# Kernel optimization log

Hardware: AMD Instinct MI355X
Metric: run time of the kernel (lower is better)

Reference implementation:

```python
import jax, jax.numpy as jnp
import numpy as np

B, S, D, T = 64, 1024, 768, 10
IS = int(S * 0.3)   # 307, token-mix inner dim
ID = int(D * 0.3)   # 230, channel-mix inner dim
EPS = 1e-5


def _cond_ln(x, embed, tid):
    # LayerNorm over last dim (no affine), then per-sample gamma/beta
    mu = jnp.mean(x, axis=-1, keepdims=True)
    var = jnp.mean(jnp.square(x - mu), axis=-1, keepdims=True)
    out = (x - mu) / jnp.sqrt(var + EPS)
    gb = embed[tid]                      # [B, 2D]
    gamma, beta = gb[:, :D], gb[:, D:]
    return gamma[:, None, :] * out + beta[:, None, :]


def setup_inputs() -> dict:
    key = jax.random.key(0)
    ks = jax.random.split(key, 8)
    x = jax.random.normal(ks[0], (B, S, D), dtype=jnp.float32)
    tasks_id = jax.random.randint(ks[1], (B,), 0, T)
    # conditional LN embeddings: gamma ~ N(1, 0.02), beta = 0
    cln1 = jnp.concatenate([1.0 + 0.02 * jax.random.normal(ks[2], (T, D)),
                            jnp.zeros((T, D))], axis=1).astype(jnp.float32)
    cln2 = jnp.concatenate([1.0 + 0.02 * jax.random.normal(ks[3], (T, D)),
                            jnp.zeros((T, D))], axis=1).astype(jnp.float32)
    # per-task weights stored [T, fout, fin] (kaiming-ish scale)
    w1_tok = jax.random.normal(ks[4], (T, IS, S), dtype=jnp.float32) * (2.0 / S) ** 0.5
    w2_tok = jax.random.normal(ks[5], (T, S, IS), dtype=jnp.float32) * (2.0 / IS) ** 0.5
    w1_ch = jax.random.normal(ks[6], (T, ID, D), dtype=jnp.float32) * (2.0 / D) ** 0.5
    w2_ch = jax.random.normal(ks[7], (T, D, ID), dtype=jnp.float32) * (2.0 / ID) ** 0.5
    return {"x": x, "tasks_id": tasks_id, "cln1": cln1, "cln2": cln2,
            "w1_tok": w1_tok, "w2_tok": w2_tok, "w1_ch": w1_ch, "w2_ch": w2_ch}


def reference(x, tasks_id, cln1, cln2, w1_tok, w2_tok, w1_ch, w2_ch):
    tid = tasks_id
    # --- token-mixing block (axis=1 ConditionalLinear) ---
    h = _cond_ln(x, cln1, tid)
    h = jnp.einsum('bnd,bcn->bcd', h, w1_tok[tid])   # [B, IS, D]
    h = jax.nn.gelu(h, approximate=False)
    h = jnp.einsum('bnd,bcn->bcd', h, w2_tok[tid])   # [B, S, D]
    x = x + h
    # --- channel-mixing block (axis=2 ConditionalLinear) ---
    h = _cond_ln(x, cln2, tid)
    h = jnp.einsum('bnd,bcd->bnc', h, w1_ch[tid])    # [B, S, ID]
    h = jax.nn.gelu(h, approximate=False)
    h = jnp.einsum('bnd,bcd->bnc', h, w2_ch[tid])    # [B, S, D]
    x = x + h
    return x
```

## Files before the change

kernel.cpp:

```cpp
#include <hip/hip_runtime.h>
#include <math.h>

typedef __bf16 bf16x8 __attribute__((ext_vector_type(8)));
typedef __bf16 bf16x4 __attribute__((ext_vector_type(4)));
typedef float  f32x4  __attribute__((ext_vector_type(4)));

constexpr int Bc = 64, Sc = 1024, Dc = 768;
constexpr int ISc = 307, IDc = 230;
constexpr int ISp = 384, IDp = 256;

static __device__ __forceinline__ float bf2f(unsigned short u) {
    return __builtin_bit_cast(float, (unsigned)u << 16);
}

static __device__ __forceinline__ void gload16(const void* g, void* l) {
    __builtin_amdgcn_global_load_lds(
        (const __attribute__((address_space(1))) void*)g,
        (__attribute__((address_space(3))) void*)l, 16, 0, 0);
}

constexpr int CH0 = 10 * ISp * (Sc  / 8);
constexpr int CH1 = 10 * Sc  * (ISp / 8);
constexpr int CH2 = 10 * IDp * (Dc  / 8);
constexpr int CH3 = 10 * Dc  * (IDp / 8);
constexpr int CB0 = CH0, CB1 = CB0 + CH1, CB2 = CB1 + CH2, CB3 = CB2 + CH3;

__device__ __forceinline__ void cvt_one(
    const float* __restrict__ in, __bf16* __restrict__ out,
    int inrows, int outrows, int incols, int outcols, int c)
{
    const int cpr  = outcols >> 3;
    const int perT = outrows * cpr;
    const int t    = c / perT;
    const int rem  = c - t * perT;
    const int r    = rem / cpr;
    const int cc   = (rem - r * cpr) * 8;
    bf16x8 o;
    if (r < inrows) {
        const float* src = in + ((long)t * inrows + r) * incols + cc;
        #pragma unroll
        for (int e = 0; e < 8; e++)
            o[e] = (cc + e < incols) ? (__bf16)src[e] : (__bf16)0.0f;
    } else {
        #pragma unroll
        for (int e = 0; e < 8; e++) o[e] = (__bf16)0.0f;
    }
    *reinterpret_cast<bf16x8*>(out + ((long)t * outrows + r) * outcols + cc) = o;
}

__global__ __launch_bounds__(256) void cvt_all(
    const float* __restrict__ w1t, const float* __restrict__ w2t,
    const float* __restrict__ w1c, const float* __restrict__ w2c,
    __bf16* __restrict__ o1t, __bf16* __restrict__ o2t,
    __bf16* __restrict__ o1c, __bf16* __restrict__ o2c)
{
    const int c = blockIdx.x * 256 + threadIdx.x;
    if (c < CB0)      cvt_one(w1t, o1t, ISc, ISp, Sc,  Sc,  c);
    else if (c < CB1) cvt_one(w2t, o2t, Sc,  Sc,  ISc, ISp, c - CB0);
    else if (c < CB2) cvt_one(w1c, o1c, IDc, IDp, Dc,  Dc,  c - CB1);
    else if (c < CB3) cvt_one(w2c, o2c, Dc,  Dc,  IDc, IDp, c - CB2);
}

__global__ __launch_bounds__(256) void ln1_t(
    const float* __restrict__ x, const int* __restrict__ tasks,
    const float* __restrict__ cln, __bf16* __restrict__ h1T)
{
    constexpr int RPB = 32, LDT = Dc + 8;
    __shared__ unsigned short T[RPB * LDT];
    const int b   = blockIdx.y;
    const int t   = tasks[b];
    const int s0  = blockIdx.x * RPB;
    const int tid = threadIdx.x;
    const int wv  = tid >> 6;
    const int l   = tid & 63;

    const float4* Ga = reinterpret_cast<const float4*>(cln + (long)t * 2 * Dc);
    const float4* Be = reinterpret_cast<const float4*>(cln + (long)t * 2 * Dc + Dc);
    const float4 g0 = Ga[l], g1 = Ga[l + 64], g2 = Ga[l + 128];
    const float4 b0 = Be[l], b1 = Be[l + 64], b2 = Be[l + 128];

    #pragma unroll
    for (int rr = 0; rr < 8; rr++) {
        const int r = wv * 8 + rr;
        const float4* xr = reinterpret_cast<const float4*>(x + ((long)b * Sc + s0 + r) * Dc);
        const float4 v0 = xr[l], v1 = xr[l + 64], v2 = xr[l + 128];
        float s = v0.x + v0.y + v0.z + v0.w + v1.x + v1.y + v1.z + v1.w
                + v2.x + v2.y + v2.z + v2.w;
        float q = v0.x*v0.x + v0.y*v0.y + v0.z*v0.z + v0.w*v0.w
                + v1.x*v1.x + v1.y*v1.y + v1.z*v1.z + v1.w*v1.w
                + v2.x*v2.x + v2.y*v2.y + v2.z*v2.z + v2.w*v2.w;
        #pragma unroll
        for (int o = 1; o < 64; o <<= 1) { s += __shfl_xor(s, o); q += __shfl_xor(q, o); }
        const float mu   = s * (1.0f / Dc);
        const float var  = fmaxf(q * (1.0f / Dc) - mu * mu, 0.0f);
        const float rstd = 1.0f / sqrtf(var + 1e-5f);
        unsigned short* tr = &T[r * LDT];
        bf16x4 o0, o1, o2;
        o0[0] = (__bf16)(g0.x * ((v0.x - mu) * rstd) + b0.x);
        o0[1] = (__bf16)(g0.y * ((v0.y - mu) * rstd) + b0.y);
        o0[2] = (__bf16)(g0.z * ((v0.z - mu) * rstd) + b0.z);
        o0[3] = (__bf16)(g0.w * ((v0.w - mu) * rstd) + b0.w);
        o1[0] = (__bf16)(g1.x * ((v1.x - mu) * rstd) + b1.x);
        o1[1] = (__bf16)(g1.y * ((v1.y - mu) * rstd) + b1.y);
        o1[2] = (__bf16)(g1.z * ((v1.z - mu) * rstd) + b1.z);
        o1[3] = (__bf16)(g1.w * ((v1.w - mu) * rstd) + b1.w);
        o2[0] = (__bf16)(g2.x * ((v2.x - mu) * rstd) + b2.x);
        o2[1] = (__bf16)(g2.y * ((v2.y - mu) * rstd) + b2.y);
        o2[2] = (__bf16)(g2.z * ((v2.z - mu) * rstd) + b2.z);
        o2[3] = (__bf16)(g2.w * ((v2.w - mu) * rstd) + b2.w);
        *reinterpret_cast<bf16x4*>(&tr[l * 4])        = o0;
        *reinterpret_cast<bf16x4*>(&tr[256 + l * 4])  = o1;
        *reinterpret_cast<bf16x4*>(&tr[512 + l * 4])  = o2;
    }
    __syncthreads();
    #pragma unroll
    for (int c = 0; c < 3; c++) {
        const int d = tid + c * 256;
        unsigned short tmp[32];
        #pragma unroll
        for (int e = 0; e < 32; e++) tmp[e] = T[e * LDT + d];
        __bf16* dst = h1T + ((long)b * Dc + d) * Sc + s0;
        #pragma unroll
        for (int u = 0; u < 4; u++)
            reinterpret_cast<uint4*>(dst)[u] = reinterpret_cast<const uint4*>(tmp)[u];
    }
}

__global__ __launch_bounds__(256) void cond_ln_b(
    const __bf16* __restrict__ x, const int* __restrict__ tasks,
    const float* __restrict__ cln, __bf16* __restrict__ out)
{
    const int row = blockIdx.x * 4 + (threadIdx.x >> 6);
    const int b   = row >> 10;
    const int t   = tasks[b];
    const int l   = threadIdx.x & 63;
    const ushort4* xr = reinterpret_cast<const ushort4*>(x + (long)row * Dc);
    const ushort4 u0 = xr[l], u1 = xr[l + 64], u2 = xr[l + 128];
    float v[12];
    v[0]=bf2f(u0.x); v[1]=bf2f(u0.y); v[2]=bf2f(u0.z); v[3]=bf2f(u0.w);
    v[4]=bf2f(u1.x); v[5]=bf2f(u1.y); v[6]=bf2f(u1.z); v[7]=bf2f(u1.w);
    v[8]=bf2f(u2.x); v[9]=bf2f(u2.y); v[10]=bf2f(u2.z); v[11]=bf2f(u2.w);
    float s = 0.f, q = 0.f;
    #pragma unroll
    for (int e = 0; e < 12; e++) { s += v[e]; q += v[e] * v[e]; }
    #pragma unroll
    for (int o = 1; o < 64; o <<= 1) { s += __shfl_xor(s, o); q += __shfl_xor(q, o); }
    const float mu   = s * (1.0f / Dc);
    const float var  = fmaxf(q * (1.0f / Dc) - mu * mu, 0.0f);
    const float rstd = 1.0f / sqrtf(var + 1e-5f);
    const float4* Ga = reinterpret_cast<const float4*>(cln + (long)t * 2 * Dc);
    const float4* Be = reinterpret_cast<const float4*>(cln + (long)t * 2 * Dc + Dc);
    ushort4* orow = reinterpret_cast<ushort4*>(out + (long)row * Dc);
    #pragma unroll
    for (int c = 0; c < 3; c++) {
        const float4 g = Ga[l + c * 64], be = Be[l + c * 64];
        bf16x4 o;
        o[0] = (__bf16)(g.x * ((v[c*4+0] - mu) * rstd) + be.x);
        o[1] = (__bf16)(g.y * ((v[c*4+1] - mu) * rstd) + be.y);
        o[2] = (__bf16)(g.z * ((v[c*4+2] - mu) * rstd) + be.z);
        o[3] = (__bf16)(g.w * ((v[c*4+3] - mu) * rstd) + be.w);
        orow[l + c * 64] = __builtin_bit_cast(ushort4, o);
    }
}

template<int DOGELU, int RESM, int OUTF32, int ATASK>
__global__ __launch_bounds__(256, 2) void gemm_tn(
    const __bf16* __restrict__ A, long sA, int lda,
    const __bf16* __restrict__ B, long sB, int ldb,
    const void* __restrict__ R, long sR,
    void* __restrict__ C, long sC, int ldc,
    const int* __restrict__ tasks, int M, int N, int K)
{
    constexpr int BM = 128, BN = 128, BK = 64;
    constexpr int BUFB = 32768;
    __shared__ uint4 lds4[2 * BUFB / 16];
    char* lbase = (char*)lds4;

    const int gx  = gridDim.x, gy = gridDim.y;
    const int tpb = gx * gy;
    const long lin = blockIdx.x + (long)gx * (blockIdx.y + (long)gy * blockIdx.z);
    const int  xcd  = (int)(lin & 7);
    const long idx  = lin >> 3;
    const int  lb   = (int)(idx / tpb);
    const int  tile = (int)(idx - (long)lb * tpb);
    const int  b    = xcd * 8 + lb;
    const int  m0   = (tile / gx) * BM;
    const int  n0   = (tile % gx) * BN;

    const int t = tasks[b];
    const __bf16* Ab = A + (ATASK ? (long)t : (long)b) * sA;
    const __bf16* Bb = B + (ATASK ? (long)b : (long)t) * sB;
    const int tid = threadIdx.x, lane = tid & 63, wid = tid >> 6;
    const int wm = (wid >> 1) * 64, wn = (wid & 1) * 64;
    const int l15 = lane & 15, l4 = lane >> 4;

    f32x4 acc[4][4];
    #pragma unroll
    for (int i = 0; i < 4; i++)
        #pragma unroll
        for (int j = 0; j < 4; j++)
            acc[i][j] = (f32x4){0.f, 0.f, 0.f, 0.f};

    auto STAGE = [&](int k0, int buf) {
        char* dst = lbase + buf * BUFB;
        #pragma unroll
        for (int rep = 0; rep < 4; rep++) {
            const int c = rep * 256 + tid;
            const int m = c >> 3, ch = c & 7;
            const int gk = k0 + ((ch ^ (m & 7)) << 3);
            gload16(Ab + (long)(m0 + m) * lda + gk, dst + c * 16);
        }
        #pragma unroll
        for (int rep = 0; rep < 4; rep++) {
            const int c = rep * 256 + tid;
            const int n = c >> 3, ch = c & 7;
            const int gk = k0 + ((ch ^ (n & 7)) << 3);
            gload16(Bb + (long)(n0 + n) * ldb + gk, dst + 16384 + c * 16);
        }
    };

    const int nt = K / BK;
    STAGE(0, 0);
    __syncthreads();
    int cur = 0;
    for (int tt = 0; tt < nt; tt++) {
        if (tt + 1 < nt) STAGE((tt + 1) * BK, cur ^ 1);
        const char* bb = lbase + cur * BUFB;
        #pragma unroll
        for (int h = 0; h < 2; h++) {
            bf16x8 af[4], bfr[4];
            #pragma unroll
            for (int i = 0; i < 4; i++) {
                const int row = wm + i * 16 + l15;
                af[i] = *reinterpret_cast<const bf16x8*>(
                    bb + row * 128 + (((h * 4 + l4) ^ (l15 & 7)) << 4));
            }
            #pragma unroll
            for (int j = 0; j < 4; j++) {
                const int row = wn + j * 16 + l15;
                bfr[j] = *reinterpret_cast<const bf16x8*>(
                    bb + 16384 + row * 128 + (((h * 4 + l4) ^ (l15 & 7)) << 4));
            }
            #pragma unroll
            for (int i = 0; i < 4; i++)
                #pragma unroll
                for (int j = 0; j < 4; j++)
                    acc[i][j] = __builtin_amdgcn_mfma_f32_16x16x32_bf16(af[i], bfr[j], acc[i][j], 0, 0, 0);
        }
        __syncthreads();
        cur ^= 1;
    }

    float*  Cf = (float*)C  + (long)b * sC;
    __bf16* Ch = (__bf16*)C + (long)b * sC;
    const float*  Rf = (RESM == 1) ? ((const float*)R  + (long)b * sR) : nullptr;
    const __bf16* Rh = (RESM == 2) ? ((const __bf16*)R + (long)b * sR) : nullptr;

    #pragma unroll
    for (int i = 0; i < 4; i++) {
        #pragma unroll
        for (int j = 0; j < 4; j++) {
            const int gn = n0 + wn + j * 16 + l15;
            #pragma unroll
            for (int r = 0; r < 4; r++) {
                const int gm = m0 + wm + i * 16 + l4 * 4 + r;
                float v = acc[i][j][r];
                if (DOGELU) v = 0.5f * v * (1.0f + erff(v * 0.70710678118654752f));
                if (RESM == 1) v += Rf[(long)gm * ldc + gn];
                if (RESM == 2) v += (float)Rh[(long)gm * ldc + gn];
                if (OUTF32) Cf[(long)gm * ldc + gn] = v;
                else        Ch[(long)gm * ldc + gn] = (__bf16)v;
            }
        }
    }
}

extern "C" void kernel_launch(void* const* d_in, const int* in_sizes, int n_in,
                              void* d_out, int out_size, void* d_ws, size_t ws_size,
                              hipStream_t stream) {
    const float* x      = (const float*)d_in[0];
    const int*   tasks  = (const int*)  d_in[1];
    const float* cln1   = (const float*)d_in[2];
    const float* cln2   = (const float*)d_in[3];
    const float* w1_tok = (const float*)d_in[4];
    const float* w2_tok = (const float*)d_in[5];
    const float* w1_ch  = (const float*)d_in[6];
    const float* w2_ch  = (const float*)d_in[7];
    float* out = (float*)d_out;

    char* ws = (char*)d_ws;
    const long oT1 = 0;
    const long oT2 = oT1 + (long)10 * ISp * Sc * 2;
    const long oC1 = oT2 + (long)10 * Sc * ISp * 2;
    const long oC2 = oC1 + (long)10 * IDp * Dc * 2;
    const long oA  = oC2 + (long)10 * Dc * IDp * 2;
    const long oG  = oA  + (long)Bc * Dc * Sc * 2;
    __bf16* wT1  = (__bf16*)(ws + oT1);
    __bf16* wT2  = (__bf16*)(ws + oT2);
    __bf16* wC1  = (__bf16*)(ws + oC1);
    __bf16* wC2  = (__bf16*)(ws + oC2);
    __bf16* h1T  = (__bf16*)(ws + oA);
    __bf16* x1   = (__bf16*)(ws + oA);
    __bf16* gbf  = (__bf16*)(ws + oG);
    __bf16* h2   = (__bf16*)d_out;

    const dim3 blk(256);
    auto cdiv = [](long a, long b) { return (int)((a + b - 1) / b); };

    cvt_all<<<cdiv(CB3, 256), blk, 0, stream>>>(
        w1_tok, w2_tok, w1_ch, w2_ch, wT1, wT2, wC1, wC2);

    ln1_t<<<dim3(Sc / 32, Bc), blk, 0, stream>>>(x, tasks, cln1, h1T);

    gemm_tn<1, 0, 0, 0><<<dim3(ISp / 128, Dc / 128, Bc), blk, 0, stream>>>(
        h1T, (long)Dc * Sc, Sc,
        wT1, (long)ISp * Sc, Sc,
        nullptr, 0,
        gbf, (long)Dc * ISp, ISp,
        tasks, Dc, ISp, Sc);

    gemm_tn<0, 1, 0, 1><<<dim3(Dc / 128, Sc / 128, Bc), blk, 0, stream>>>(
        wT2, (long)Sc * ISp, ISp,
        gbf, (long)Dc * ISp, ISp,
        x, (long)Sc * Dc,
        x1, (long)Sc * Dc, Dc,
        tasks, Sc, Dc, ISp);

    cond_ln_b<<<(Bc * Sc) / 4, blk, 0, stream>>>(x1, tasks, cln2, h2);

    gemm_tn<1, 0, 0, 0><<<dim3(IDp / 128, Sc / 128, Bc), blk, 0, stream>>>(
        h2, (long)Sc * Dc, Dc,
        wC1, (long)IDp * Dc, Dc,
        nullptr, 0,
        gbf, (long)Sc * IDp, IDp,
        tasks, Sc, IDp, Dc);

    gemm_tn<0, 2, 1, 0><<<dim3(Dc / 128, Sc / 128, Bc), blk, 0, stream>>>(
        gbf, (long)Sc * IDp, IDp,
        wC2, (long)Dc * IDp, IDp,
        x1, (long)Sc * Dc,
        out, (long)Sc * Dc, Dc,
        tasks, Sc, Dc, IDp);
}
```

Before: 461.3 us.

## Fuse channel-mix LayerNorm, both GEMMs, GELU and residual into one kernel

```diff
diff --git a/kernel.cpp b/kernel.cpp
--- a/kernel.cpp
+++ b/kernel.cpp
@@ -11,6 +11,9 @@
 
 static __device__ __forceinline__ float bf2f(unsigned short u) {
     return __builtin_bit_cast(float, (unsigned)u << 16);
+}
+static __device__ __forceinline__ float gelu_f(float v) {
+    return 0.5f * v * (1.0f + erff(v * 0.70710678118654752f));
 }
 
 static __device__ __forceinline__ void gload16(const void* g, void* l) {
@@ -126,43 +129,6 @@
     }
 }
 
-__global__ __launch_bounds__(256) void cond_ln_b(
-    const __bf16* __restrict__ x, const int* __restrict__ tasks,
-    const float* __restrict__ cln, __bf16* __restrict__ out)
-{
-    const int row = blockIdx.x * 4 + (threadIdx.x >> 6);
-    const int b   = row >> 10;
-    const int t   = tasks[b];
-    const int l   = threadIdx.x & 63;
-    const ushort4* xr = reinterpret_cast<const ushort4*>(x + (long)row * Dc);
-    const ushort4 u0 = xr[l], u1 = xr[l + 64], u2 = xr[l + 128];
-    float v[12];
-    v[0]=bf2f(u0.x); v[1]=bf2f(u0.y); v[2]=bf2f(u0.z); v[3]=bf2f(u0.w);
-    v[4]=bf2f(u1.x); v[5]=bf2f(u1.y); v[6]=bf2f(u1.z); v[7]=bf2f(u1.w);
-    v[8]=bf2f(u2.x); v[9]=bf2f(u2.y); v[10]=bf2f(u2.z); v[11]=bf2f(u2.w);
-    float s = 0.f, q = 0.f;
-    #pragma unroll
-    for (int e = 0; e < 12; e++) { s += v[e]; q += v[e] * v[e]; }
-    #pragma unroll
-    for (int o = 1; o < 64; o <<= 1) { s += __shfl_xor(s, o); q += __shfl_xor(q, o); }
-    const float mu   = s * (1.0f / Dc);
-    const float var  = fmaxf(q * (1.0f / Dc) - mu * mu, 0.0f);
-    const float rstd = 1.0f / sqrtf(var + 1e-5f);
-    const float4* Ga = reinterpret_cast<const float4*>(cln + (long)t * 2 * Dc);
-    const float4* Be = reinterpret_cast<const float4*>(cln + (long)t * 2 * Dc + Dc);
-    ushort4* orow = reinterpret_cast<ushort4*>(out + (long)row * Dc);
-    #pragma unroll
-    for (int c = 0; c < 3; c++) {
-        const float4 g = Ga[l + c * 64], be = Be[l + c * 64];
-        bf16x4 o;
-        o[0] = (__bf16)(g.x * ((v[c*4+0] - mu) * rstd) + be.x);
-        o[1] = (__bf16)(g.y * ((v[c*4+1] - mu) * rstd) + be.y);
-        o[2] = (__bf16)(g.z * ((v[c*4+2] - mu) * rstd) + be.z);
-        o[3] = (__bf16)(g.w * ((v[c*4+3] - mu) * rstd) + be.w);
-        orow[l + c * 64] = __builtin_bit_cast(ushort4, o);
-    }
-}
-
 template<int DOGELU, int RESM, int OUTF32, int ATASK>
 __global__ __launch_bounds__(256, 2) void gemm_tn(
     const __bf16* __restrict__ A, long sA, int lda,
@@ -233,13 +199,13 @@
             for (int i = 0; i < 4; i++) {
                 const int row = wm + i * 16 + l15;
                 af[i] = *reinterpret_cast<const bf16x8*>(
-                    bb + row * 128 + (((h * 4 + l4) ^ (l15 & 7)) << 4));
+                    bb + row * 128 + (((h * 4 + l4) ^ (row & 7)) << 4));
             }
             #pragma unroll
             for (int j = 0; j < 4; j++) {
                 const int row = wn + j * 16 + l15;
                 bfr[j] = *reinterpret_cast<const bf16x8*>(
-                    bb + 16384 + row * 128 + (((h * 4 + l4) ^ (l15 & 7)) << 4));
+                    bb + 16384 + row * 128 + (((h * 4 + l4) ^ (row & 7)) << 4));
             }
             #pragma unroll
             for (int i = 0; i < 4; i++)
@@ -265,11 +231,223 @@
             for (int r = 0; r < 4; r++) {
                 const int gm = m0 + wm + i * 16 + l4 * 4 + r;
                 float v = acc[i][j][r];
-                if (DOGELU) v = 0.5f * v * (1.0f + erff(v * 0.70710678118654752f));
+                if (DOGELU) v = gelu_f(v);
                 if (RESM == 1) v += Rf[(long)gm * ldc + gn];
                 if (RESM == 2) v += (float)Rh[(long)gm * ldc + gn];
                 if (OUTF32) Cf[(long)gm * ldc + gn] = v;
                 else        Ch[(long)gm * ldc + gn] = (__bf16)v;
+            }
+        }
+    }
+}
+
+__global__ __launch_bounds__(512, 1) void mlp_ch(
+    const __bf16* __restrict__ x1, const int* __restrict__ tasks,
+    const float* __restrict__ cln2,
+    const __bf16* __restrict__ wC1,
+    const __bf16* __restrict__ wC2,
+    float* __restrict__ out)
+{
+    __shared__ float2 st[128];
+    __shared__ unsigned short G[128 * 256];
+    __shared__ char sbuf[2][32768];
+
+    const int lin = blockIdx.x;
+    const int xcd = lin & 7;
+    const int idx = lin >> 3;
+    const int b   = xcd * 8 + (idx >> 3);
+    const int m0  = (idx & 7) * 128;
+    const int t   = tasks[b];
+
+    const int tid = threadIdx.x;
+    const int wid = tid >> 6, lane = tid & 63;
+    const int g   = wid >> 2, wid2 = wid & 3;
+    const int wm  = (wid2 >> 1) * 64, wn = (wid2 & 1) * 64;
+    const int l15 = lane & 15, l4 = lane >> 4;
+
+    const __bf16* xb = x1 + ((long)b * Sc + m0) * Dc;
+    const float*  cg = cln2 + (long)t * 2 * Dc;
+    const float*  cb = cg + Dc;
+
+    #pragma unroll 2
+    for (int rr = 0; rr < 16; rr++) {
+        const int m = wid * 16 + rr;
+        const ushort4* xr = reinterpret_cast<const ushort4*>(xb + (long)m * Dc);
+        const ushort4 u0 = xr[lane], u1 = xr[lane + 64], u2 = xr[lane + 128];
+        float s = 0.f, q = 0.f, v;
+        v = bf2f(u0.x); s += v; q += v*v;  v = bf2f(u0.y); s += v; q += v*v;
+        v = bf2f(u0.z); s += v; q += v*v;  v = bf2f(u0.w); s += v; q += v*v;
+        v = bf2f(u1.x); s += v; q += v*v;  v = bf2f(u1.y); s += v; q += v*v;
+        v = bf2f(u1.z); s += v; q += v*v;  v = bf2f(u1.w); s += v; q += v*v;
+        v = bf2f(u2.x); s += v; q += v*v;  v = bf2f(u2.y); s += v; q += v*v;
+        v = bf2f(u2.z); s += v; q += v*v;  v = bf2f(u2.w); s += v; q += v*v;
+        #pragma unroll
+        for (int o = 1; o < 64; o <<= 1) { s += __shfl_xor(s, o); q += __shfl_xor(q, o); }
+        if (lane == 0) {
+            const float mu  = s * (1.0f / Dc);
+            const float var = fmaxf(q * (1.0f / Dc) - mu * mu, 0.0f);
+            st[m] = make_float2(mu, 1.0f / sqrtf(var + 1e-5f));
+        }
+    }
+    __syncthreads();
+
+    const int am = tid >> 2, ach = tid & 3;
+    const float2 ams = st[am];
+    const __bf16* arow = xb + (long)am * Dc;
+
+    auto loadA = [&](int kt) -> bf16x8 {
+        return *reinterpret_cast<const bf16x8*>(arow + kt * 32 + ach * 8);
+    };
+    auto writeA = [&](bf16x8 a, int buf) {
+        const int gk = 0;  (void)gk;
+        *reinterpret_cast<bf16x8*>(sbuf[buf] + am * 64 + ((ach ^ (am & 3)) << 4)) = a;
+    };
+    auto stageB1 = [&](int kt, int buf) {
+        #pragma unroll
+        for (int rep = 0; rep < 2; rep++) {
+            const int c = rep * 512 + tid;
+            const int n = c >> 2, ch = c & 3;
+            const int gk = kt * 32 + ((ch ^ (n & 3)) << 3);
+            gload16(wC1 + ((long)t * IDp + n) * Dc + gk, sbuf[buf] + 8192 + c * 16);
+        }
+    };
+    auto xformA = [&](bf16x8 raw, int kt) -> bf16x8 {
+        const int gk = kt * 32 + ach * 8;
+        const float4 ga0 = reinterpret_cast<const float4*>(cg + gk)[0];
+        const float4 ga1 = reinterpret_cast<const float4*>(cg + gk)[1];
+        const float4 be0 = reinterpret_cast<const float4*>(cb + gk)[0];
+        const float4 be1 = reinterpret_cast<const float4*>(cb + gk)[1];
+        bf16x8 o;
+        o[0] = (__bf16)(ga0.x * ((float)raw[0] - ams.x) * ams.y + be0.x);
+        o[1] = (__bf16)(ga0.y * ((float)raw[1] - ams.x) * ams.y + be0.y);
+        o[2] = (__bf16)(ga0.z * ((float)raw[2] - ams.x) * ams.y + be0.z);
+        o[3] = (__bf16)(ga0.w * ((float)raw[3] - ams.x) * ams.y + be0.w);
+        o[4] = (__bf16)(ga1.x * ((float)raw[4] - ams.x) * ams.y + be1.x);
+        o[5] = (__bf16)(ga1.y * ((float)raw[5] - ams.x) * ams.y + be1.y);
+        o[6] = (__bf16)(ga1.z * ((float)raw[6] - ams.x) * ams.y + be1.z);
+        o[7] = (__bf16)(ga1.w * ((float)raw[7] - ams.x) * ams.y + be1.w);
+        return o;
+    };
+
+    f32x4 acc[4][4];
+    #pragma unroll
+    for (int i = 0; i < 4; i++)
+        #pragma unroll
+        for (int j = 0; j < 4; j++)
+            acc[i][j] = (f32x4){0.f, 0.f, 0.f, 0.f};
+
+    {
+        bf16x8 a0 = loadA(0);
+        stageB1(0, 0);
+        writeA(xformA(a0, 0), 0);
+        __syncthreads();
+        for (int kt = 0; kt < 24; kt++) {
+            const int buf = kt & 1;
+            bf16x8 anx;
+            if (kt < 23) { anx = loadA(kt + 1); stageB1(kt + 1, buf ^ 1); }
+            const char* Abase = sbuf[buf];
+            const char* Bbase = sbuf[buf] + 8192;
+            bf16x8 af[4], bfr[4];
+            #pragma unroll
+            for (int i = 0; i < 4; i++) {
+                const int row = wm + i * 16 + l15;
+                af[i] = *reinterpret_cast<const bf16x8*>(
+                    Abase + row * 64 + ((l4 ^ (row & 3)) << 4));
+            }
+            #pragma unroll
+            for (int j = 0; j < 4; j++) {
+                const int row = g * 128 + wn + j * 16 + l15;
+                bfr[j] = *reinterpret_cast<const bf16x8*>(
+                    Bbase + row * 64 + ((l4 ^ (row & 3)) << 4));
+            }
+            #pragma unroll
+            for (int i = 0; i < 4; i++)
+                #pragma unroll
+                for (int j = 0; j < 4; j++)
+                    acc[i][j] = __builtin_amdgcn_mfma_f32_16x16x32_bf16(af[i], bfr[j], acc[i][j], 0, 0, 0);
+            if (kt < 23) writeA(xformA(anx, kt + 1), buf ^ 1);
+            __syncthreads();
+        }
+    }
+
+    #pragma unroll
+    for (int i = 0; i < 4; i++) {
+        #pragma unroll
+        for (int j = 0; j < 4; j++) {
+            const int k = g * 128 + wn + j * 16 + l15;
+            #pragma unroll
+            for (int r = 0; r < 4; r++) {
+                const int m = wm + i * 16 + l4 * 4 + r;
+                const float v = gelu_f(acc[i][j][r]);
+                const int chunk = k >> 3;
+                const int phys  = chunk ^ (m & 7);
+                G[m * 256 + phys * 8 + (k & 7)] =
+                    __builtin_bit_cast(unsigned short, (__bf16)v);
+            }
+        }
+    }
+    __syncthreads();
+
+    const __bf16* w2b = wC2 + (long)t * Dc * IDp;
+    for (int nc = 0; nc < 3; nc++) {
+        auto stageB2 = [&](int kt, int buf) {
+            #pragma unroll
+            for (int rep = 0; rep < 4; rep++) {
+                const int c = rep * 512 + tid;
+                const int n = c >> 3, ch = c & 7;
+                const int gk = kt * 64 + ((ch ^ (n & 7)) << 3);
+                gload16(w2b + (long)(nc * 256 + n) * IDp + gk, sbuf[buf] + c * 16);
+            }
+        };
+        f32x4 a2[4][4];
+        #pragma unroll
+        for (int i = 0; i < 4; i++)
+            #pragma unroll
+            for (int j = 0; j < 4; j++)
+                a2[i][j] = (f32x4){0.f, 0.f, 0.f, 0.f};
+
+        stageB2(0, 0);
+        __syncthreads();
+        for (int kt = 0; kt < 4; kt++) {
+            const int buf = kt & 1;
+            if (kt < 3) stageB2(kt + 1, buf ^ 1);
+            #pragma unroll
+            for (int h = 0; h < 2; h++) {
+                bf16x8 af[4], bfr[4];
+                #pragma unroll
+                for (int i = 0; i < 4; i++) {
+                    const int row = wm + i * 16 + l15;
+                    const int chunk = kt * 8 + h * 4 + l4;
+                    const int phys  = chunk ^ (row & 7);
+                    af[i] = *reinterpret_cast<const bf16x8*>(
+                        (const char*)G + row * 512 + phys * 16);
+                }
+                #pragma unroll
+                for (int j = 0; j < 4; j++) {
+                    const int row = g * 128 + wn + j * 16 + l15;
+                    bfr[j] = *reinterpret_cast<const bf16x8*>(
+                        sbuf[buf] + row * 128 + (((h * 4 + l4) ^ (row & 7)) << 4));
+                }
+                #pragma unroll
+                for (int i = 0; i < 4; i++)
+                    #pragma unroll
+                    for (int j = 0; j < 4; j++)
+                        a2[i][j] = __builtin_amdgcn_mfma_f32_16x16x32_bf16(af[i], bfr[j], a2[i][j], 0, 0, 0);
+            }
+            __syncthreads();
+        }
+        float* ob = out + ((long)b * Sc + m0) * Dc;
+        #pragma unroll
+        for (int i = 0; i < 4; i++) {
+            #pragma unroll
+            for (int j = 0; j < 4; j++) {
+                const int gn = nc * 256 + g * 128 + wn + j * 16 + l15;
+                #pragma unroll
+                for (int r = 0; r < 4; r++) {
+                    const int gm = wm + i * 16 + l4 * 4 + r;
+                    ob[(long)gm * Dc + gn] =
+                        a2[i][j][r] + (float)xb[(long)gm * Dc + gn];
+                }
             }
         }
     }
@@ -302,7 +480,6 @@
     __bf16* h1T  = (__bf16*)(ws + oA);
     __bf16* x1   = (__bf16*)(ws + oA);
     __bf16* gbf  = (__bf16*)(ws + oG);
-    __bf16* h2   = (__bf16*)d_out;
 
     const dim3 blk(256);
     auto cdiv = [](long a, long b) { return (int)((a + b - 1) / b); };
@@ -326,19 +503,5 @@
         x1, (long)Sc * Dc, Dc,
         tasks, Sc, Dc, ISp);
 
-    cond_ln_b<<<(Bc * Sc) / 4, blk, 0, stream>>>(x1, tasks, cln2, h2);
-
-    gemm_tn<1, 0, 0, 0><<<dim3(IDp / 128, Sc / 128, Bc), blk, 0, stream>>>(
-        h2, (long)Sc * Dc, Dc,
-        wC1, (long)IDp * Dc, Dc,
-        nullptr, 0,
-        gbf, (long)Sc * IDp, IDp,
-        tasks, Sc, IDp, Dc);
-
-    gemm_tn<0, 2, 1, 0><<<dim3(Dc / 128, Sc / 128, Bc), blk, 0, stream>>>(
-        gbf, (long)Sc * IDp, IDp,
-        wC2, (long)Dc * IDp, IDp,
-        x1, (long)Sc * Dc,
-        out, (long)Sc * Dc, Dc,
-        tasks, Sc, Dc, IDp);
-}
+    mlp_ch<<<(Sc / 128) * Bc, 512, 0, stream>>>(x1, tasks, cln2, wC1, wC2, out);
+}
```

After: 451.4 us. 1.02x faster.
